# Performance work log

Measured on AMD Instinct MI355X. Metric: run time of the kernel, lower is better.

Reference implementation:

```python
import jax, jax.numpy as jnp
import numpy as np

B, T, F_DIM, H_DIM = 1024, 128, 128, 512


def setup_inputs() -> dict:
    key = jax.random.key(0)
    ks = jax.random.split(key, 20)
    s_f = 1.0 / np.sqrt(F_DIM)
    s_h = 1.0 / np.sqrt(H_DIM)
    s_2f = 1.0 / np.sqrt(2 * F_DIM)
    return {
        "X": jax.random.normal(ks[0], (B, T, F_DIM), jnp.float32),
        "missing_mask": jax.random.randint(ks[1], (B, T, F_DIM), 0, 2).astype(jnp.float32),
        "deltas": jax.random.uniform(ks[2], (B, T, F_DIM), jnp.float32),
        "W_gh": jax.random.normal(ks[3], (H_DIM, F_DIM), jnp.float32) * s_f,
        "b_gh": jax.random.normal(ks[4], (H_DIM,), jnp.float32) * s_f,
        "W_gx": jax.random.normal(ks[5], (F_DIM, F_DIM), jnp.float32) * s_f,
        "b_gx": jax.random.normal(ks[6], (F_DIM,), jnp.float32) * s_f,
        "W_hist": jax.random.normal(ks[7], (F_DIM, H_DIM), jnp.float32) * s_h,
        "b_hist": jax.random.normal(ks[8], (F_DIM,), jnp.float32) * s_h,
        "W_feat": jax.random.normal(ks[9], (F_DIM, F_DIM), jnp.float32) * s_f,
        "b_feat": jax.random.normal(ks[10], (F_DIM,), jnp.float32) * s_f,
        "W_comb": jax.random.normal(ks[11], (F_DIM, 2 * F_DIM), jnp.float32) * s_2f,
        "b_comb": jax.random.normal(ks[12], (F_DIM,), jnp.float32) * s_2f,
        "W_ih": jax.random.normal(ks[13], (4 * H_DIM, 2 * F_DIM), jnp.float32) * s_h,
        "W_hh": jax.random.normal(ks[14], (4 * H_DIM, H_DIM), jnp.float32) * s_h,
        "b_ih": jax.random.normal(ks[15], (4 * H_DIM,), jnp.float32) * s_h,
        "b_hh": jax.random.normal(ks[16], (4 * H_DIM,), jnp.float32) * s_h,
    }


def _rits(X, missing_mask, deltas, W_gh, b_gh, W_gx, b_gx, W_hist, b_hist,
          W_feat, b_feat, W_comb, b_comb, W_ih, W_hh, b_ih, b_hh):
    f = X.shape[-1]
    eye = jnp.eye(f, dtype=X.dtype)
    Wgx_diag = W_gx * eye          # TemporalDecay(diag=True) masks W with identity
    Wfeat_od = W_feat * (1.0 - eye)

    def step(carry, xs):
        h, c = carry
        x, m, d = xs  # each [B, F]
        gamma_h = jnp.exp(-jax.nn.relu(d @ W_gh.T + b_gh))      # [B, H]
        gamma_x = jnp.exp(-jax.nn.relu(d @ Wgx_diag.T + b_gx))  # [B, F]
        h = h * gamma_h
        x_h = h @ W_hist.T + b_hist
        x_c = m * x + (1.0 - m) * x_h
        z_h = x_c @ Wfeat_od.T + b_feat
        alpha = jax.nn.sigmoid(jnp.concatenate([gamma_x, m], -1) @ W_comb.T + b_comb)
        c_h = alpha * z_h + (1.0 - alpha) * x_h
        c_c = m * x + (1.0 - m) * c_h
        inp = jnp.concatenate([c_c, m], -1)  # [B, 2F]
        gates = inp @ W_ih.T + b_ih + h @ W_hh.T + b_hh  # [B, 4H]
        i_g, f_g, g_g, o_g = jnp.split(gates, 4, axis=-1)
        c_new = jax.nn.sigmoid(f_g) * c + jax.nn.sigmoid(i_g) * jnp.tanh(g_g)
        h_new = jax.nn.sigmoid(o_g) * jnp.tanh(c_new)
        return (h_new, c_new), (x_h, z_h, c_h)

    b = X.shape[0]
    hdim = W_gh.shape[0]
    h0 = jnp.zeros((b, hdim), X.dtype)
    c0 = jnp.zeros((b, hdim), X.dtype)
    xs = (jnp.swapaxes(X, 0, 1), jnp.swapaxes(missing_mask, 0, 1), jnp.swapaxes(deltas, 0, 1))
    (h_T, _), (XH, ZH, CH) = jax.lax.scan(step, (h0, c0), xs)
    XH = jnp.swapaxes(XH, 0, 1)
    ZH = jnp.swapaxes(ZH, 0, 1)
    CH = jnp.swapaxes(CH, 0, 1)  # reconstruction == stacked c_h
    imputed = missing_mask * X + (1.0 - missing_mask) * CH
    return imputed, CH, h_T, XH, CH, ZH


def reference(X, missing_mask, deltas, W_gh, b_gh, W_gx, b_gx, W_hist, b_hist,
              W_feat, b_feat, W_comb, b_comb, W_ih, W_hh, b_ih, b_hh):
    return _rits(X, missing_mask, deltas, W_gh, b_gh, W_gx, b_gx, W_hist, b_hist,
                 W_feat, b_feat, W_comb, b_comb, W_ih, W_hh, b_ih, b_hh)
```

## Files before the change

### kernel.cpp

```cpp
#include <hip/hip_runtime.h>
#include <math.h>

#define B_ 1024
#define T_ 128
#define F_ 128
#define H_ 512

#define O_IMP 0
#define O_CH1 16777216
#define O_HT  33554432
#define O_XH  34078720
#define O_CH2 50855936
#define O_ZH  67633152

__device__ __forceinline__ float sigm(float x) { return 1.0f / (1.0f + __expf(-x)); }

__global__ __launch_bounds__(256) void init_state(float* ws) {
  int i = blockIdx.x * 256 + threadIdx.x;
  const int n = (B_ * H_) / 4;
  float4 z = make_float4(0.f, 0.f, 0.f, 0.f);
  float4* w4 = (float4*)ws;
  if (i < n) w4[i] = z;
  else       w4[i + n] = z;
}

__global__ __launch_bounds__(256) void rits_phaseA(
    const float* __restrict__ X, const float* __restrict__ MM, const float* __restrict__ D,
    const float* __restrict__ W_gx, const float* __restrict__ b_gx,
    const float* __restrict__ W_hist, const float* __restrict__ b_hist,
    const float* __restrict__ W_feat, const float* __restrict__ b_feat,
    const float* __restrict__ W_comb, const float* __restrict__ b_comb,
    const float* __restrict__ hdec, float* __restrict__ cc_ws,
    float* __restrict__ out, int t)
{
  __shared__ float hds[4][516];
  __shared__ float wch[128][68];
  __shared__ float xcs[4][132];
  __shared__ float gxm[4][260];

  const int tid = threadIdx.x;
  const int f = tid & 127;
  const int rp = tid >> 7;
  const int r0 = blockIdx.x * 4;

  #pragma unroll
  for (int i = 0; i < 2; ++i) {
    int f4 = tid + 256 * i;
    int row = f4 >> 7, c4 = f4 & 127;
    *(float4*)&hds[row][c4 * 4] = *(const float4*)&hdec[(r0 + row) * H_ + c4 * 4];
  }
  __syncthreads();

  float xh[2];
  { float bh = b_hist[f]; xh[0] = xh[1] = bh; }
  for (int kc = 0; kc < 8; ++kc) {
    int k0 = kc * 64;
    #pragma unroll
    for (int i = 0; i < 8; ++i) {
      int f4 = tid + 256 * i;
      int row = f4 >> 4, c4 = f4 & 15;
      *(float4*)&wch[row][c4 * 4] = *(const float4*)&W_hist[row * H_ + k0 + c4 * 4];
    }
    __syncthreads();
    #pragma unroll 4
    for (int k = 0; k < 64; k += 4) {
      float4 w = *(const float4*)&wch[f][k];
      #pragma unroll
      for (int i = 0; i < 2; ++i) {
        float4 h4 = *(const float4*)&hds[rp * 2 + i][k0 + k];
        xh[i] += w.x * h4.x + w.y * h4.y + w.z * h4.z + w.w * h4.w;
      }
    }
    __syncthreads();
  }

  float xv[2], mv[2], xcv[2];
  {
    float wgx = W_gx[f * F_ + f];
    float bgx = b_gx[f];
    #pragma unroll
    for (int i = 0; i < 2; ++i) {
      int r = rp * 2 + i;
      int idx = ((r0 + r) * T_ + t) * F_ + f;
      float x = X[idx], m = MM[idx], d = D[idx];
      xv[i] = x; mv[i] = m;
      float xc = m * x + (1.f - m) * xh[i];
      xcv[i] = xc;
      xcs[r][f] = xc;
      gxm[r][f] = __expf(-fmaxf(d * wgx + bgx, 0.f));
      gxm[r][F_ + f] = m;
      out[O_XH + idx] = xh[i];
    }
  }
  __syncthreads();

  float zh[2];
  {
    float wff = W_feat[f * F_ + f];
    float bf = b_feat[f];
    #pragma unroll
    for (int i = 0; i < 2; ++i) zh[i] = bf - xcv[i] * wff;
  }
  for (int kc = 0; kc < 2; ++kc) {
    int k0 = kc * 64;
    #pragma unroll
    for (int i = 0; i < 8; ++i) {
      int f4 = tid + 256 * i;
      int row = f4 >> 4, c4 = f4 & 15;
      *(float4*)&wch[row][c4 * 4] = *(const float4*)&W_feat[row * F_ + k0 + c4 * 4];
    }
    __syncthreads();
    #pragma unroll 4
    for (int k = 0; k < 64; k += 4) {
      float4 w = *(const float4*)&wch[f][k];
      #pragma unroll
      for (int i = 0; i < 2; ++i) {
        float4 c4v = *(const float4*)&xcs[rp * 2 + i][k0 + k];
        zh[i] += w.x * c4v.x + w.y * c4v.y + w.z * c4v.z + w.w * c4v.w;
      }
    }
    __syncthreads();
  }

  float al[2];
  { float bcb = b_comb[f];
    #pragma unroll
    for (int i = 0; i < 2; ++i) al[i] = bcb; }
  for (int kc = 0; kc < 4; ++kc) {
    int k0 = kc * 64;
    #pragma unroll
    for (int i = 0; i < 8; ++i) {
      int f4 = tid + 256 * i;
      int row = f4 >> 4, c4 = f4 & 15;
      *(float4*)&wch[row][c4 * 4] = *(const float4*)&W_comb[row * 256 + k0 + c4 * 4];
    }
    __syncthreads();
    #pragma unroll 4
    for (int k = 0; k < 64; k += 4) {
      float4 w = *(const float4*)&wch[f][k];
      #pragma unroll
      for (int i = 0; i < 2; ++i) {
        float4 g4 = *(const float4*)&gxm[rp * 2 + i][k0 + k];
        al[i] += w.x * g4.x + w.y * g4.y + w.z * g4.z + w.w * g4.w;
      }
    }
    __syncthreads();
  }

  #pragma unroll
  for (int i = 0; i < 2; ++i) {
    int r = rp * 2 + i;
    int idx = ((r0 + r) * T_ + t) * F_ + f;
    float a = sigm(al[i]);
    float ch = a * zh[i] + (1.f - a) * xh[i];
    float cc = mv[i] * xv[i] + (1.f - mv[i]) * ch;
    out[O_IMP + idx] = cc;
    out[O_CH1 + idx] = ch;
    out[O_CH2 + idx] = ch;
    out[O_ZH  + idx] = zh[i];
    cc_ws[(r0 + r) * F_ + f] = cc;
  }
}

__global__ __launch_bounds__(256) void rits_phaseB(
    const float* __restrict__ MM, const float* __restrict__ D,
    const float* __restrict__ W_gh, const float* __restrict__ b_gh,
    const float* __restrict__ W_ih, const float* __restrict__ W_hh,
    const float* __restrict__ b_ih, const float* __restrict__ b_hh,
    const float* __restrict__ cc_ws, const float* __restrict__ hdec_in,
    float* __restrict__ hdec_out, float* __restrict__ c_ws,
    float* __restrict__ out, int t)
{
  __shared__ float Ash[32][68];
  __shared__ float Wsh[32][132];
  __shared__ float gsh[64][132];
  __shared__ float wgsh[32][132];

  const int tid = threadIdx.x;
  const int tx = tid & 31, ty = tid >> 5;
  const int r0 = blockIdx.x * 64;
  const int c0 = blockIdx.y * 32;

  #pragma unroll
  for (int i = 0; i < 4; ++i) {
    int f4 = tid + 256 * i;
    int hr = f4 >> 5, c4 = f4 & 31;
    *(float4*)&wgsh[hr][c4 * 4] = *(const float4*)&W_gh[(c0 + hr) * F_ + c4 * 4];
  }

  float acc[8][4];
  #pragma unroll
  for (int i = 0; i < 8; ++i)
    #pragma unroll
    for (int j = 0; j < 4; ++j) acc[i][j] = 0.f;

  for (int kc = 0; kc < 24; ++kc) {
    const int k0 = kc * 32;
    {
      int r = tid >> 2;
      int kq = (tid & 3) * 8;
      float4 v0, v1;
      if (k0 < 128) {
        const float* p = &cc_ws[(r0 + r) * F_ + k0 + kq];
        v0 = *(const float4*)p; v1 = *(const float4*)(p + 4);
      } else if (k0 < 256) {
        const float* p = &MM[((r0 + r) * T_ + t) * F_ + (k0 - 128) + kq];
        v0 = *(const float4*)p; v1 = *(const float4*)(p + 4);
      } else {
        const float* p = &hdec_in[(r0 + r) * H_ + (k0 - 256) + kq];
        v0 = *(const float4*)p; v1 = *(const float4*)(p + 4);
      }
      float at[8] = {v0.x, v0.y, v0.z, v0.w, v1.x, v1.y, v1.z, v1.w};
      #pragma unroll
      for (int j = 0; j < 8; ++j) Ash[kq + j][r] = at[j];
    }
    {
      int col = tid >> 1;
      int kq = (tid & 1) * 16;
      int g = (col >> 5) * H_ + c0 + (col & 31);
      const float* p = (k0 < 256) ? &W_ih[g * 256 + k0 + kq]
                                  : &W_hh[g * H_ + (k0 - 256) + kq];
      float4 w0 = *(const float4*)p;
      float4 w1 = *(const float4*)(p + 4);
      float4 w2 = *(const float4*)(p + 8);
      float4 w3 = *(const float4*)(p + 12);
      float wt[16] = {w0.x, w0.y, w0.z, w0.w, w1.x, w1.y, w1.z, w1.w,
                      w2.x, w2.y, w2.z, w2.w, w3.x, w3.y, w3.z, w3.w};
      #pragma unroll
      for (int j = 0; j < 16; ++j) Wsh[kq + j][col] = wt[j];
    }
    __syncthreads();
    #pragma unroll 4
    for (int kk = 0; kk < 32; ++kk) {
      const float4 a0 = *(const float4*)&Ash[kk][8 * ty];
      const float4 a1 = *(const float4*)&Ash[kk][8 * ty + 4];
      const float4 w  = *(const float4*)&Wsh[kk][4 * tx];
      const float av[8] = {a0.x, a0.y, a0.z, a0.w, a1.x, a1.y, a1.z, a1.w};
      #pragma unroll
      for (int i = 0; i < 8; ++i) {
        acc[i][0] = fmaf(av[i], w.x, acc[i][0]);
        acc[i][1] = fmaf(av[i], w.y, acc[i][1]);
        acc[i][2] = fmaf(av[i], w.z, acc[i][2]);
        acc[i][3] = fmaf(av[i], w.w, acc[i][3]);
      }
    }
    __syncthreads();
  }

  #pragma unroll
  for (int j = 0; j < 4; ++j) {
    int cl = 4 * tx + j;
    int g = (cl >> 5) * H_ + c0 + (cl & 31);
    float bia = b_ih[g] + b_hh[g];
    #pragma unroll
    for (int i = 0; i < 8; ++i) gsh[8 * ty + i][cl] = acc[i][j] + bia;
  }
  __syncthreads();

  const int hl = tid & 31;
  const int rg = tid >> 5;
  float hnew[8];
  #pragma unroll
  for (int i = 0; i < 8; ++i) {
    int r = 8 * rg + i;
    float ig = gsh[r][hl];
    float fg = gsh[r][32 + hl];
    float gg = gsh[r][64 + hl];
    float og = gsh[r][96 + hl];
    int cidx = (r0 + r) * H_ + c0 + hl;
    float cn = sigm(fg) * c_ws[cidx] + sigm(ig) * tanhf(gg);
    c_ws[cidx] = cn;
    hnew[i] = sigm(og) * tanhf(cn);
  }
  __syncthreads();

  if (t == T_ - 1) {
    #pragma unroll
    for (int i = 0; i < 8; ++i) {
      int r = 8 * rg + i;
      out[O_HT + (r0 + r) * H_ + c0 + hl] = hnew[i];
    }
  } else {
    #pragma unroll
    for (int i = 0; i < 8; ++i) {
      int f4 = tid + 256 * i;
      int r = f4 >> 5, c4 = f4 & 31;
      *(float4*)&gsh[r][c4 * 4] = *(const float4*)&D[((r0 + r) * T_ + (t + 1)) * F_ + c4 * 4];
    }
    __syncthreads();
    float bg = b_gh[c0 + hl];
    float dot0[8];
    #pragma unroll
    for (int i = 0; i < 8; ++i) dot0[i] = 0.f;
    for (int kb = 0; kb < 128; kb += 16) {
      const float4 w0 = *(const float4*)&wgsh[hl][kb];
      const float4 w1 = *(const float4*)&wgsh[hl][kb + 4];
      const float4 w2 = *(const float4*)&wgsh[hl][kb + 8];
      const float4 w3 = *(const float4*)&wgsh[hl][kb + 12];
      #pragma unroll
      for (int i = 0; i < 8; ++i) {
        const float* dr = &gsh[8 * rg + i][kb];
        const float4 d0 = *(const float4*)dr;
        const float4 d1 = *(const float4*)(dr + 4);
        const float4 d2 = *(const float4*)(dr + 8);
        const float4 d3 = *(const float4*)(dr + 12);
        dot0[i] += w0.x * d0.x + w0.y * d0.y + w0.z * d0.z + w0.w * d0.w
                 + w1.x * d1.x + w1.y * d1.y + w1.z * d1.z + w1.w * d1.w
                 + w2.x * d2.x + w2.y * d2.y + w2.z * d2.z + w2.w * d2.w
                 + w3.x * d3.x + w3.y * d3.y + w3.z * d3.z + w3.w * d3.w;
      }
    }
    #pragma unroll
    for (int i = 0; i < 8; ++i) {
      int r = 8 * rg + i;
      float gam = __expf(-fmaxf(dot0[i] + bg, 0.f));
      hdec_out[(r0 + r) * H_ + c0 + hl] = hnew[i] * gam;
    }
  }
}

extern "C" void kernel_launch(void* const* d_in, const int* in_sizes, int n_in,
                              void* d_out, int out_size, void* d_ws, size_t ws_size,
                              hipStream_t stream) {
  const float* X      = (const float*)d_in[0];
  const float* MM     = (const float*)d_in[1];
  const float* D      = (const float*)d_in[2];
  const float* W_gh   = (const float*)d_in[3];
  const float* b_gh   = (const float*)d_in[4];
  const float* W_gx   = (const float*)d_in[5];
  const float* b_gx   = (const float*)d_in[6];
  const float* W_hist = (const float*)d_in[7];
  const float* b_hist = (const float*)d_in[8];
  const float* W_feat = (const float*)d_in[9];
  const float* b_feat = (const float*)d_in[10];
  const float* W_comb = (const float*)d_in[11];
  const float* b_comb = (const float*)d_in[12];
  const float* W_ih   = (const float*)d_in[13];
  const float* W_hh   = (const float*)d_in[14];
  const float* b_ih   = (const float*)d_in[15];
  const float* b_hh   = (const float*)d_in[16];

  float* out = (float*)d_out;
  float* ws = (float*)d_ws;
  float* hd0 = ws;
  float* hd1 = ws + B_ * H_;
  float* cst = ws + 2 * B_ * H_;
  float* ccb = ws + 3 * B_ * H_;

  init_state<<<dim3(1024), dim3(256), 0, stream>>>(ws);

  for (int t = 0; t < T_; ++t) {
    float* hin  = (t & 1) ? hd1 : hd0;
    float* hout = (t & 1) ? hd0 : hd1;
    rits_phaseA<<<dim3(256), dim3(256), 0, stream>>>(
        X, MM, D, W_gx, b_gx, W_hist, b_hist, W_feat, b_feat, W_comb, b_comb,
        hin, ccb, out, t);
    rits_phaseB<<<dim3(16, 16), dim3(256), 0, stream>>>(
        MM, D, W_gh, b_gh, W_ih, W_hh, b_ih, b_hh,
        ccb, hin, hout, cst, out, t);
  }
}
```

Measured before the change: 13.01 ms.

## Double threads per block and register-prefetch next weight tiles in both phases

Both per-timestep kernels now launch 512 threads per block, so each thread computes half as many rows (phase A: one row per thread, phase B: a 4x4 micro-tile instead of 8x4). Each K-chunk loop now loads the next chunk's weights and activations into registers while the current shared-memory tile is being consumed, which hides global-load latency behind the FMA loop. The aim is more active waves per CU and overlap of memory with compute in a launch-bound recurrent loop. In exchange there is less work per thread, so register-level reuse in the phase-B GEMM drops and more shared-memory traffic is spent per FMA.

```diff
diff --git a/kernel.cpp b/kernel.cpp
--- a/kernel.cpp
+++ b/kernel.cpp
@@ -24,7 +24,7 @@
   else       w4[i + n] = z;
 }
 
-__global__ __launch_bounds__(256) void rits_phaseA(
+__global__ __launch_bounds__(512) void rits_phaseA(
     const float* __restrict__ X, const float* __restrict__ MM, const float* __restrict__ D,
     const float* __restrict__ W_gx, const float* __restrict__ b_gx,
     const float* __restrict__ W_hist, const float* __restrict__ b_hist,
@@ -43,126 +43,145 @@
   const int rp = tid >> 7;
   const int r0 = blockIdx.x * 4;
 
-  #pragma unroll
-  for (int i = 0; i < 2; ++i) {
-    int f4 = tid + 256 * i;
-    int row = f4 >> 7, c4 = f4 & 127;
+  const int swrow[1] = {0};  (void)swrow;
+
+  {
+    int row = tid >> 7, c4 = tid & 127;
     *(float4*)&hds[row][c4 * 4] = *(const float4*)&hdec[(r0 + row) * H_ + c4 * 4];
   }
-  __syncthreads();
-
-  float xh[2];
-  { float bh = b_hist[f]; xh[0] = xh[1] = bh; }
+
+  float xh = b_hist[f];
+  float4 pw[4];
+  #pragma unroll
+  for (int i = 0; i < 4; ++i) {
+    int f4 = tid + 512 * i;
+    int row = f4 >> 4, c4 = f4 & 15;
+    pw[i] = *(const float4*)&W_hist[row * H_ + 0 + c4 * 4];
+  }
   for (int kc = 0; kc < 8; ++kc) {
+    #pragma unroll
+    for (int i = 0; i < 4; ++i) {
+      int f4 = tid + 512 * i;
+      int row = f4 >> 4, c4 = f4 & 15;
+      *(float4*)&wch[row][c4 * 4] = pw[i];
+    }
+    __syncthreads();
+    if (kc < 7) {
+      int k0 = (kc + 1) * 64;
+      #pragma unroll
+      for (int i = 0; i < 4; ++i) {
+        int f4 = tid + 512 * i;
+        int row = f4 >> 4, c4 = f4 & 15;
+        pw[i] = *(const float4*)&W_hist[row * H_ + k0 + c4 * 4];
+      }
+    }
     int k0 = kc * 64;
-    #pragma unroll
-    for (int i = 0; i < 8; ++i) {
-      int f4 = tid + 256 * i;
-      int row = f4 >> 4, c4 = f4 & 15;
-      *(float4*)&wch[row][c4 * 4] = *(const float4*)&W_hist[row * H_ + k0 + c4 * 4];
-    }
-    __syncthreads();
     #pragma unroll 4
     for (int k = 0; k < 64; k += 4) {
       float4 w = *(const float4*)&wch[f][k];
-      #pragma unroll
-      for (int i = 0; i < 2; ++i) {
-        float4 h4 = *(const float4*)&hds[rp * 2 + i][k0 + k];
-        xh[i] += w.x * h4.x + w.y * h4.y + w.z * h4.z + w.w * h4.w;
-      }
-    }
-    __syncthreads();
-  }
-
-  float xv[2], mv[2], xcv[2];
+      float4 h4 = *(const float4*)&hds[rp][k0 + k];
+      xh += w.x * h4.x + w.y * h4.y + w.z * h4.z + w.w * h4.w;
+    }
+    __syncthreads();
+  }
+
+  float xv, mv, xcv;
   {
     float wgx = W_gx[f * F_ + f];
     float bgx = b_gx[f];
-    #pragma unroll
-    for (int i = 0; i < 2; ++i) {
-      int r = rp * 2 + i;
-      int idx = ((r0 + r) * T_ + t) * F_ + f;
-      float x = X[idx], m = MM[idx], d = D[idx];
-      xv[i] = x; mv[i] = m;
-      float xc = m * x + (1.f - m) * xh[i];
-      xcv[i] = xc;
-      xcs[r][f] = xc;
-      gxm[r][f] = __expf(-fmaxf(d * wgx + bgx, 0.f));
-      gxm[r][F_ + f] = m;
-      out[O_XH + idx] = xh[i];
-    }
+    int idx = ((r0 + rp) * T_ + t) * F_ + f;
+    float x = X[idx], m = MM[idx], d = D[idx];
+    xv = x; mv = m;
+    float xc = m * x + (1.f - m) * xh;
+    xcv = xc;
+    xcs[rp][f] = xc;
+    gxm[rp][f] = __expf(-fmaxf(d * wgx + bgx, 0.f));
+    gxm[rp][F_ + f] = m;
+    out[O_XH + idx] = xh;
   }
   __syncthreads();
 
-  float zh[2];
-  {
-    float wff = W_feat[f * F_ + f];
-    float bf = b_feat[f];
-    #pragma unroll
-    for (int i = 0; i < 2; ++i) zh[i] = bf - xcv[i] * wff;
+  float zh = b_feat[f] - xcv * W_feat[f * F_ + f];
+  #pragma unroll
+  for (int i = 0; i < 4; ++i) {
+    int f4 = tid + 512 * i;
+    int row = f4 >> 4, c4 = f4 & 15;
+    pw[i] = *(const float4*)&W_feat[row * F_ + 0 + c4 * 4];
   }
   for (int kc = 0; kc < 2; ++kc) {
+    #pragma unroll
+    for (int i = 0; i < 4; ++i) {
+      int f4 = tid + 512 * i;
+      int row = f4 >> 4, c4 = f4 & 15;
+      *(float4*)&wch[row][c4 * 4] = pw[i];
+    }
+    __syncthreads();
+    if (kc < 1) {
+      #pragma unroll
+      for (int i = 0; i < 4; ++i) {
+        int f4 = tid + 512 * i;
+        int row = f4 >> 4, c4 = f4 & 15;
+        pw[i] = *(const float4*)&W_feat[row * F_ + 64 + c4 * 4];
+      }
+    }
     int k0 = kc * 64;
-    #pragma unroll
-    for (int i = 0; i < 8; ++i) {
-      int f4 = tid + 256 * i;
-      int row = f4 >> 4, c4 = f4 & 15;
-      *(float4*)&wch[row][c4 * 4] = *(const float4*)&W_feat[row * F_ + k0 + c4 * 4];
-    }
-    __syncthreads();
     #pragma unroll 4
     for (int k = 0; k < 64; k += 4) {
       float4 w = *(const float4*)&wch[f][k];
-      #pragma unroll
-      for (int i = 0; i < 2; ++i) {
-        float4 c4v = *(const float4*)&xcs[rp * 2 + i][k0 + k];
-        zh[i] += w.x * c4v.x + w.y * c4v.y + w.z * c4v.z + w.w * c4v.w;
-      }
-    }
-    __syncthreads();
-  }
-
-  float al[2];
-  { float bcb = b_comb[f];
-    #pragma unroll
-    for (int i = 0; i < 2; ++i) al[i] = bcb; }
+      float4 c4v = *(const float4*)&xcs[rp][k0 + k];
+      zh += w.x * c4v.x + w.y * c4v.y + w.z * c4v.z + w.w * c4v.w;
+    }
+    __syncthreads();
+  }
+
+  float al = b_comb[f];
+  #pragma unroll
+  for (int i = 0; i < 4; ++i) {
+    int f4 = tid + 512 * i;
+    int row = f4 >> 4, c4 = f4 & 15;
+    pw[i] = *(const float4*)&W_comb[row * 256 + 0 + c4 * 4];
+  }
   for (int kc = 0; kc < 4; ++kc) {
+    #pragma unroll
+    for (int i = 0; i < 4; ++i) {
+      int f4 = tid + 512 * i;
+      int row = f4 >> 4, c4 = f4 & 15;
+      *(float4*)&wch[row][c4 * 4] = pw[i];
+    }
+    __syncthreads();
+    if (kc < 3) {
+      int k0 = (kc + 1) * 64;
+      #pragma unroll
+      for (int i = 0; i < 4; ++i) {
+        int f4 = tid + 512 * i;
+        int row = f4 >> 4, c4 = f4 & 15;
+        pw[i] = *(const float4*)&W_comb[row * 256 + k0 + c4 * 4];
+      }
+    }
     int k0 = kc * 64;
-    #pragma unroll
-    for (int i = 0; i < 8; ++i) {
-      int f4 = tid + 256 * i;
-      int row = f4 >> 4, c4 = f4 & 15;
-      *(float4*)&wch[row][c4 * 4] = *(const float4*)&W_comb[row * 256 + k0 + c4 * 4];
-    }
-    __syncthreads();
     #pragma unroll 4
     for (int k = 0; k < 64; k += 4) {
       float4 w = *(const float4*)&wch[f][k];
-      #pragma unroll
-      for (int i = 0; i < 2; ++i) {
-        float4 g4 = *(const float4*)&gxm[rp * 2 + i][k0 + k];
-        al[i] += w.x * g4.x + w.y * g4.y + w.z * g4.z + w.w * g4.w;
-      }
-    }
-    __syncthreads();
-  }
-
-  #pragma unroll
-  for (int i = 0; i < 2; ++i) {
-    int r = rp * 2 + i;
-    int idx = ((r0 + r) * T_ + t) * F_ + f;
-    float a = sigm(al[i]);
-    float ch = a * zh[i] + (1.f - a) * xh[i];
-    float cc = mv[i] * xv[i] + (1.f - mv[i]) * ch;
+      float4 g4 = *(const float4*)&gxm[rp][k0 + k];
+      al += w.x * g4.x + w.y * g4.y + w.z * g4.z + w.w * g4.w;
+    }
+    __syncthreads();
+  }
+
+  {
+    int idx = ((r0 + rp) * T_ + t) * F_ + f;
+    float a = sigm(al);
+    float ch = a * zh + (1.f - a) * xh;
+    float cc = mv * xv + (1.f - mv) * ch;
     out[O_IMP + idx] = cc;
     out[O_CH1 + idx] = ch;
     out[O_CH2 + idx] = ch;
-    out[O_ZH  + idx] = zh[i];
-    cc_ws[(r0 + r) * F_ + f] = cc;
+    out[O_ZH  + idx] = zh;
+    cc_ws[(r0 + rp) * F_ + f] = cc;
   }
 }
 
-__global__ __launch_bounds__(256) void rits_phaseB(
+__global__ __launch_bounds__(512) void rits_phaseB(
     const float* __restrict__ MM, const float* __restrict__ D,
     const float* __restrict__ W_gh, const float* __restrict__ b_gh,
     const float* __restrict__ W_ih, const float* __restrict__ W_hh,
@@ -182,62 +201,58 @@
   const int c0 = blockIdx.y * 32;
 
   #pragma unroll
-  for (int i = 0; i < 4; ++i) {
-    int f4 = tid + 256 * i;
+  for (int i = 0; i < 2; ++i) {
+    int f4 = tid + 512 * i;
     int hr = f4 >> 5, c4 = f4 & 31;
     *(float4*)&wgsh[hr][c4 * 4] = *(const float4*)&W_gh[(c0 + hr) * F_ + c4 * 4];
   }
 
-  float acc[8][4];
-  #pragma unroll
-  for (int i = 0; i < 8; ++i)
+  const int ar = tid >> 3;
+  const int akq = (tid & 7) * 4;
+  const int wcol = tid >> 2;
+  const int wkq = (tid & 3) * 8;
+  const int wg = (wcol >> 5) * H_ + c0 + (wcol & 31);
+
+  float4 pa, pw0, pw1;
+  {
+    pa = *(const float4*)&cc_ws[(r0 + ar) * F_ + akq];
+    const float* q = &W_ih[wg * 256 + wkq];
+    pw0 = *(const float4*)q; pw1 = *(const float4*)(q + 4);
+  }
+
+  float acc[4][4];
+  #pragma unroll
+  for (int i = 0; i < 4; ++i)
     #pragma unroll
     for (int j = 0; j < 4; ++j) acc[i][j] = 0.f;
 
   for (int kc = 0; kc < 24; ++kc) {
-    const int k0 = kc * 32;
     {
-      int r = tid >> 2;
-      int kq = (tid & 3) * 8;
-      float4 v0, v1;
-      if (k0 < 128) {
-        const float* p = &cc_ws[(r0 + r) * F_ + k0 + kq];
-        v0 = *(const float4*)p; v1 = *(const float4*)(p + 4);
-      } else if (k0 < 256) {
-        const float* p = &MM[((r0 + r) * T_ + t) * F_ + (k0 - 128) + kq];
-        v0 = *(const float4*)p; v1 = *(const float4*)(p + 4);
-      } else {
-        const float* p = &hdec_in[(r0 + r) * H_ + (k0 - 256) + kq];
-        v0 = *(const float4*)p; v1 = *(const float4*)(p + 4);
-      }
-      float at[8] = {v0.x, v0.y, v0.z, v0.w, v1.x, v1.y, v1.z, v1.w};
-      #pragma unroll
-      for (int j = 0; j < 8; ++j) Ash[kq + j][r] = at[j];
-    }
-    {
-      int col = tid >> 1;
-      int kq = (tid & 1) * 16;
-      int g = (col >> 5) * H_ + c0 + (col & 31);
-      const float* p = (k0 < 256) ? &W_ih[g * 256 + k0 + kq]
-                                  : &W_hh[g * H_ + (k0 - 256) + kq];
-      float4 w0 = *(const float4*)p;
-      float4 w1 = *(const float4*)(p + 4);
-      float4 w2 = *(const float4*)(p + 8);
-      float4 w3 = *(const float4*)(p + 12);
-      float wt[16] = {w0.x, w0.y, w0.z, w0.w, w1.x, w1.y, w1.z, w1.w,
-                      w2.x, w2.y, w2.z, w2.w, w3.x, w3.y, w3.z, w3.w};
-      #pragma unroll
-      for (int j = 0; j < 16; ++j) Wsh[kq + j][col] = wt[j];
-    }
-    __syncthreads();
+      Ash[akq + 0][ar] = pa.x; Ash[akq + 1][ar] = pa.y;
+      Ash[akq + 2][ar] = pa.z; Ash[akq + 3][ar] = pa.w;
+      float wt[8] = {pw0.x, pw0.y, pw0.z, pw0.w, pw1.x, pw1.y, pw1.z, pw1.w};
+      #pragma unroll
+      for (int j = 0; j < 8; ++j) Wsh[wkq + j][wcol] = wt[j];
+    }
+    __syncthreads();
+    if (kc < 23) {
+      int k0 = (kc + 1) * 32;
+      const float* p;
+      if (k0 < 128)      p = &cc_ws[(r0 + ar) * F_ + k0 + akq];
+      else if (k0 < 256) p = &MM[((r0 + ar) * T_ + t) * F_ + (k0 - 128) + akq];
+      else               p = &hdec_in[(r0 + ar) * H_ + (k0 - 256) + akq];
+      pa = *(const float4*)p;
+      const float* q = (k0 < 256) ? &W_ih[wg * 256 + k0 + wkq]
+                                  : &W_hh[wg * H_ + (k0 - 256) + wkq];
+      pw0 = *(const float4*)q; pw1 = *(const float4*)(q + 4);
+    }
     #pragma unroll 4
     for (int kk = 0; kk < 32; ++kk) {
-      const float4 a0 = *(const float4*)&Ash[kk][8 * ty];
-      const float4 a1 = *(const float4*)&Ash[kk][8 * ty + 4];
-      const float4 w  = *(const float4*)&Wsh[kk][4 * tx];
-      const float av[8] = {a0.x, a0.y, a0.z, a0.w, a1.x, a1.y, a1.z, a1.w};
-      #pragma unroll
-      for (int i = 0; i < 8; ++i) {
+      const float4 a = *(const float4*)&Ash[kk][4 * ty];
+      const float4 w = *(const float4*)&Wsh[kk][4 * tx];
+      const float av[4] = {a.x, a.y, a.z, a.w};
+      #pragma unroll
+      for (int i = 0; i < 4; ++i) {
         acc[i][0] = fmaf(av[i], w.x, acc[i][0]);
         acc[i][1] = fmaf(av[i], w.y, acc[i][1]);
         acc[i][2] = fmaf(av[i], w.z, acc[i][2]);
@@ -253,16 +268,16 @@
     int g = (cl >> 5) * H_ + c0 + (cl & 31);
     float bia = b_ih[g] + b_hh[g];
     #pragma unroll
-    for (int i = 0; i < 8; ++i) gsh[8 * ty + i][cl] = acc[i][j] + bia;
+    for (int i = 0; i < 4; ++i) gsh[4 * ty + i][cl] = acc[i][j] + bia;
   }
   __syncthreads();
 
   const int hl = tid & 31;
   const int rg = tid >> 5;
-  float hnew[8];
-  #pragma unroll
-  for (int i = 0; i < 8; ++i) {
-    int r = 8 * rg + i;
+  float hnew[4];
+  #pragma unroll
+  for (int i = 0; i < 4; ++i) {
+    int r = 4 * rg + i;
     float ig = gsh[r][hl];
     float fg = gsh[r][32 + hl];
     float gg = gsh[r][64 + hl];
@@ -276,30 +291,30 @@
 
   if (t == T_ - 1) {
     #pragma unroll
-    for (int i = 0; i < 8; ++i) {
-      int r = 8 * rg + i;
+    for (int i = 0; i < 4; ++i) {
+      int r = 4 * rg + i;
       out[O_HT + (r0 + r) * H_ + c0 + hl] = hnew[i];
     }
   } else {
     #pragma unroll
-    for (int i = 0; i < 8; ++i) {
-      int f4 = tid + 256 * i;
+    for (int i = 0; i < 4; ++i) {
+      int f4 = tid + 512 * i;
       int r = f4 >> 5, c4 = f4 & 31;
       *(float4*)&gsh[r][c4 * 4] = *(const float4*)&D[((r0 + r) * T_ + (t + 1)) * F_ + c4 * 4];
     }
     __syncthreads();
     float bg = b_gh[c0 + hl];
-    float dot0[8];
-    #pragma unroll
-    for (int i = 0; i < 8; ++i) dot0[i] = 0.f;
+    float dot0[4];
+    #pragma unroll
+    for (int i = 0; i < 4; ++i) dot0[i] = 0.f;
     for (int kb = 0; kb < 128; kb += 16) {
       const float4 w0 = *(const float4*)&wgsh[hl][kb];
       const float4 w1 = *(const float4*)&wgsh[hl][kb + 4];
       const float4 w2 = *(const float4*)&wgsh[hl][kb + 8];
       const float4 w3 = *(const float4*)&wgsh[hl][kb + 12];
       #pragma unroll
-      for (int i = 0; i < 8; ++i) {
-        const float* dr = &gsh[8 * rg + i][kb];
+      for (int i = 0; i < 4; ++i) {
+        const float* dr = &gsh[4 * rg + i][kb];
         const float4 d0 = *(const float4*)dr;
         const float4 d1 = *(const float4*)(dr + 4);
         const float4 d2 = *(const float4*)(dr + 8);
@@ -311,8 +326,8 @@
       }
     }
     #pragma unroll
-    for (int i = 0; i < 8; ++i) {
-      int r = 8 * rg + i;
+    for (int i = 0; i < 4; ++i) {
+      int r = 4 * rg + i;
       float gam = __expf(-fmaxf(dot0[i] + bg, 0.f));
       hdec_out[(r0 + r) * H_ + c0 + hl] = hnew[i] * gam;
     }
@@ -352,10 +367,10 @@
   for (int t = 0; t < T_; ++t) {
     float* hin  = (t & 1) ? hd1 : hd0;
     float* hout = (t & 1) ? hd0 : hd1;
-    rits_phaseA<<<dim3(256), dim3(256), 0, stream>>>(
+    rits_phaseA<<<dim3(256), dim3(512), 0, stream>>>(
         X, MM, D, W_gx, b_gx, W_hist, b_hist, W_feat, b_feat, W_comb, b_comb,
         hin, ccb, out, t);
-    rits_phaseB<<<dim3(16, 16), dim3(256), 0, stream>>>(
+    rits_phaseB<<<dim3(16, 16), dim3(512), 0, stream>>>(
         MM, D, W_gh, b_gh, W_ih, W_hh, b_ih, b_hh,
         ccb, hin, hout, cst, out, t);
   }
```

Result: no change. 13.04 ms (+0.3%).
